# Optimization experiments

Measured on AMD Instinct MI355X. Metric: run time of the kernel, lower is better.

## Reference

```python
import jax, jax.numpy as jnp
import numpy as np

EPS = 1e-12


def setup_inputs() -> dict:
    key = jax.random.key(0)
    B, T, F = 16, 3000, 513
    hop, fs, t_psd = 256, 16000, 0.1
    alpha = jnp.array([1.0 - np.exp(-(hop / fs) / t_psd)], dtype=jnp.float32)
    x = jax.random.normal(key, (B, T, F), dtype=jnp.float32)
    running_mean = jnp.zeros((1, 1, F), dtype=jnp.float32)
    running_var = jnp.ones((1, 1, F), dtype=jnp.float32)
    return {"x": x, "running_mean": running_mean, "running_var": running_var, "alpha": alpha}


def reference(x, running_mean, running_var, alpha):
    # x: (B, T, F). EMA mean/var recurrence over T, then normalize.
    a = alpha.reshape(())
    B, T, F = x.shape
    m0 = jnp.broadcast_to(running_mean[:, 0, :], (B, F))
    v0 = jnp.broadcast_to(running_var[:, 0, :], (B, F))
    xt = jnp.swapaxes(x, 0, 1)  # (T, B, F)

    def step(carry, frame):
        m, v = carry
        m = (1.0 - a) * m + a * frame
        v = (1.0 - a) * v + a * (frame - m) ** 2
        return (m, v), (m, v)

    _, (means, vars_) = jax.lax.scan(step, (m0, v0), xt)
    means = jnp.swapaxes(means, 0, 1)  # (B, T, F)
    vars_ = jnp.swapaxes(vars_, 0, 1)
    return (x - means) / (vars_ * 4.0 + EPS)
```

## Files before the change

### kernel.cpp

```cpp
#include <hip/hip_runtime.h>


#define EPS 1e-12f

constexpr int B = 16;
constexpr int T = 3000;
constexpr int F = 513;
constexpr int CHUNK = 40;
constexpr int WARM = 64;
constexpr int NC = T / CHUNK;
constexpr int BT = 8;

__global__ __launch_bounds__(256, 8)
void OnlineNorm_11982958756550_kernel(
    const float* __restrict__ x,
    const float* __restrict__ rmean,
    const float* __restrict__ rvar,
    const float* __restrict__ alpha_p,
    float* __restrict__ out)
{
    const int idx = blockIdx.x * 256 + threadIdx.x;
    if (idx >= B * F) return;
    const int c = blockIdx.y;
    const int f = idx % F;
    const int b = idx / F;

    const float a = alpha_p[0];
    const float om_a = 1.0f - a;

    const int w_start = c * CHUNK;
    int t0 = w_start - WARM;
    float m, v;
    if (t0 <= 0) { t0 = 0; m = rmean[f]; v = rvar[f]; }
    else         { m = 0.0f; v = 0.0f; }

    const int nrows = w_start + CHUNK - t0;
    const int nb = nrows / BT;
    const int wb = (w_start - t0) / BT;

    const size_t cs = (size_t)BT * F;
    const float* lp = x   + (size_t)b * T * F + (size_t)t0 * F + f;
    const float* lend = lp + (size_t)nb * cs;
    float*       op = out + (size_t)b * T * F + (size_t)w_start * F + f;

    float bufA[BT], bufB[BT];

    #pragma unroll
    for (int i = 0; i < BT; ++i) bufA[i] = lp[(size_t)i * F];
    lp += cs;
    if (nb > 1) {
        #pragma unroll
        for (int i = 0; i < BT; ++i) bufB[i] = lp[(size_t)i * F];
        lp += cs;
    }

    auto process = [&](float (&buf)[BT], int k) {
        const bool is_out = (k >= wb);
        float r[BT];
        #pragma unroll
        for (int i = 0; i < BT; ++i) {
            const float e = buf[i] - m;
            m = fmaf(a, e, m);
            const float d = e * om_a;
            v = fmaf(a, fmaf(d, d, -v), v);
            if (is_out)
                r[i] = d * __builtin_amdgcn_rcpf(fmaf(v, 4.0f, EPS));
        }
        if (lp < lend) {
            #pragma unroll
            for (int i = 0; i < BT; ++i) buf[i] = lp[(size_t)i * F];
            lp += cs;
        }
        if (is_out) {
            #pragma unroll
            for (int i = 0; i < BT; ++i) op[(size_t)i * F] = r[i];
            op += cs;
        }
    };

    int k = 0;
    while (k < nb) {
        process(bufA, k); ++k;
        if (k >= nb) break;
        process(bufB, k); ++k;
    }
}

extern "C" void kernel_launch(void* const* d_in, const int* in_sizes, int n_in,
                              void* d_out, int out_size, void* d_ws, size_t ws_size,
                              hipStream_t stream) {
    const float* x      = (const float*)d_in[0];
    const float* rmean  = (const float*)d_in[1];
    const float* rvar   = (const float*)d_in[2];
    const float* alpha  = (const float*)d_in[3];
    float* out = (float*)d_out;

    const int bf = B * F;
    dim3 block(256);
    dim3 grid((bf + 255) / 256, NC);
    OnlineNorm_11982958756550_kernel<<<grid, block, 0, stream>>>(
        x, rmean, rvar, alpha, out);
}
```

Before: 208.3 us.

## Vectorize EMA normalization so each thread handles four features with 128-bit accesses

Remaps the kernel so each block covers one batch row and each of 128 threads processes four adjacent features through 16-byte loads and stores. The last thread also handles the leftover 513th feature as a scalar. Launch bounds and grid shape change to match. The aim is fewer memory instructions and more independent recurrences per thread, at the cost of far fewer resident threads for latency hiding, possibly unaligned vector accesses since F is odd, and extra serial work on the tail thread.

```diff
diff --git a/kernel.cpp b/kernel.cpp
--- a/kernel.cpp
+++ b/kernel.cpp
@@ -11,7 +11,16 @@
 constexpr int NC = T / CHUNK;
 constexpr int BT = 8;
 
-__global__ __launch_bounds__(256, 8)
+struct V4 { float v[4]; };
+
+__device__ __forceinline__ V4 ld4(const float* p) {
+    V4 r; __builtin_memcpy(&r, p, sizeof(V4)); return r;
+}
+__device__ __forceinline__ void st4(float* p, const V4& x) {
+    __builtin_memcpy(p, &x, sizeof(V4));
+}
+
+__global__ __launch_bounds__(128, 3)
 void OnlineNorm_11982958756550_kernel(
     const float* __restrict__ x,
     const float* __restrict__ rmean,
@@ -19,70 +28,113 @@
     const float* __restrict__ alpha_p,
     float* __restrict__ out)
 {
-    const int idx = blockIdx.x * 256 + threadIdx.x;
-    if (idx >= B * F) return;
+    const int b = blockIdx.x;
+    const int r = threadIdx.x;
+    const int f0 = r * 4;
+    const bool tail = (r == 127);
     const int c = blockIdx.y;
-    const int f = idx % F;
-    const int b = idx / F;
 
     const float a = alpha_p[0];
     const float om_a = 1.0f - a;
 
     const int w_start = c * CHUNK;
     int t0 = w_start - WARM;
-    float m, v;
-    if (t0 <= 0) { t0 = 0; m = rmean[f]; v = rvar[f]; }
-    else         { m = 0.0f; v = 0.0f; }
+    float m[4], v[4], ms, vs;
+    if (t0 <= 0) {
+        t0 = 0;
+        const V4 mm = ld4(rmean + f0);
+        const V4 vv = ld4(rvar + f0);
+        #pragma unroll
+        for (int j = 0; j < 4; ++j) { m[j] = mm.v[j]; v[j] = vv.v[j]; }
+        ms = rmean[F - 1]; vs = rvar[F - 1];
+    } else {
+        #pragma unroll
+        for (int j = 0; j < 4; ++j) { m[j] = 0.0f; v[j] = 0.0f; }
+        ms = 0.0f; vs = 0.0f;
+    }
 
     const int nrows = w_start + CHUNK - t0;
     const int nb = nrows / BT;
     const int wb = (w_start - t0) / BT;
 
     const size_t cs = (size_t)BT * F;
-    const float* lp = x   + (size_t)b * T * F + (size_t)t0 * F + f;
+    const size_t colbase = (size_t)b * T * F;
+    const float* lp   = x   + colbase + (size_t)t0 * F + f0;
+    const float* tlp  = x   + colbase + (size_t)t0 * F + (F - 1);
+    float*       op   = out + colbase + (size_t)w_start * F + f0;
+    float*       top  = out + colbase + (size_t)w_start * F + (F - 1);
     const float* lend = lp + (size_t)nb * cs;
-    float*       op = out + (size_t)b * T * F + (size_t)w_start * F + f;
 
-    float bufA[BT], bufB[BT];
+    V4 bufA[BT], bufB[BT];
+    float tbA[BT], tbB[BT];
 
     #pragma unroll
-    for (int i = 0; i < BT; ++i) bufA[i] = lp[(size_t)i * F];
-    lp += cs;
-    if (nb > 1) {
+    for (int i = 0; i < BT; ++i) bufA[i] = ld4(lp + (size_t)i * F);
+    if (tail) {
         #pragma unroll
-        for (int i = 0; i < BT; ++i) bufB[i] = lp[(size_t)i * F];
-        lp += cs;
+        for (int i = 0; i < BT; ++i) tbA[i] = tlp[(size_t)i * F];
     }
+    lp += cs; tlp += cs;
 
-    auto process = [&](float (&buf)[BT], int k) {
+    #pragma unroll
+    for (int i = 0; i < BT; ++i) bufB[i] = ld4(lp + (size_t)i * F);
+    if (tail) {
+        #pragma unroll
+        for (int i = 0; i < BT; ++i) tbB[i] = tlp[(size_t)i * F];
+    }
+    lp += cs; tlp += cs;
+
+    auto process = [&](V4 (&buf)[BT], float (&tb)[BT], int k) {
         const bool is_out = (k >= wb);
-        float r[BT];
+        V4 rr[BT]; float rt[BT];
         #pragma unroll
         for (int i = 0; i < BT; ++i) {
-            const float e = buf[i] - m;
-            m = fmaf(a, e, m);
-            const float d = e * om_a;
-            v = fmaf(a, fmaf(d, d, -v), v);
-            if (is_out)
-                r[i] = d * __builtin_amdgcn_rcpf(fmaf(v, 4.0f, EPS));
+            #pragma unroll
+            for (int j = 0; j < 4; ++j) {
+                const float e = buf[i].v[j] - m[j];
+                m[j] = fmaf(a, e, m[j]);
+                const float d = e * om_a;
+                v[j] = fmaf(a, fmaf(d, d, -v[j]), v[j]);
+                if (is_out)
+                    rr[i].v[j] = d * __builtin_amdgcn_rcpf(fmaf(v[j], 4.0f, EPS));
+            }
+        }
+        if (tail) {
+            #pragma unroll
+            for (int i = 0; i < BT; ++i) {
+                const float e = tb[i] - ms;
+                ms = fmaf(a, e, ms);
+                const float d = e * om_a;
+                vs = fmaf(a, fmaf(d, d, -vs), vs);
+                if (is_out)
+                    rt[i] = d * __builtin_amdgcn_rcpf(fmaf(vs, 4.0f, EPS));
+            }
         }
         if (lp < lend) {
             #pragma unroll
-            for (int i = 0; i < BT; ++i) buf[i] = lp[(size_t)i * F];
-            lp += cs;
+            for (int i = 0; i < BT; ++i) buf[i] = ld4(lp + (size_t)i * F);
+            if (tail) {
+                #pragma unroll
+                for (int i = 0; i < BT; ++i) tb[i] = tlp[(size_t)i * F];
+            }
+            lp += cs; tlp += cs;
         }
         if (is_out) {
             #pragma unroll
-            for (int i = 0; i < BT; ++i) op[(size_t)i * F] = r[i];
-            op += cs;
+            for (int i = 0; i < BT; ++i) st4(op + (size_t)i * F, rr[i]);
+            if (tail) {
+                #pragma unroll
+                for (int i = 0; i < BT; ++i) top[(size_t)i * F] = rt[i];
+            }
+            op += cs; top += cs;
         }
     };
 
     int k = 0;
     while (k < nb) {
-        process(bufA, k); ++k;
+        process(bufA, tbA, k); ++k;
         if (k >= nb) break;
-        process(bufB, k); ++k;
+        process(bufB, tbB, k); ++k;
     }
 }
 
@@ -95,9 +147,8 @@
     const float* alpha  = (const float*)d_in[3];
     float* out = (float*)d_out;
 
-    const int bf = B * F;
-    dim3 block(256);
-    dim3 grid((bf + 255) / 256, NC);
+    dim3 block(128);
+    dim3 grid(B, NC);
     OnlineNorm_11982958756550_kernel<<<grid, block, 0, stream>>>(
         x, rmean, rvar, alpha, out);
 }
```

New measurement: 223.2 us. 1.07x slower.

## Stage time-tiles through double-buffered LDS with one block per batch-chunk

Applied to the files above, without the earlier changes.

Each block now handles one (batch, chunk) pair. A tile of 8 frames x 513 features is staged into double-buffered shared memory using aligned float4 global loads, and each thread then runs the EMA recurrence for two features, plus the last feature on thread 255. This is meant to replace the unaligned strided per-thread loads with wide coalesced ones, and to overlap the next tile's fetch with compute. In exchange, the grid has about half as many blocks, each thread carries a longer serial chain, every step needs a block-wide barrier, and thread 255 does extra serial work. Launch bounds are relaxed to 4 blocks per SM.

```diff
diff --git a/kernel.cpp b/kernel.cpp
--- a/kernel.cpp
+++ b/kernel.cpp
@@ -10,8 +10,9 @@
 constexpr int WARM = 64;
 constexpr int NC = T / CHUNK;
 constexpr int BT = 8;
+constexpr int BWF = BT * F;
 
-__global__ __launch_bounds__(256, 8)
+__global__ __launch_bounds__(256, 4)
 void OnlineNorm_11982958756550_kernel(
     const float* __restrict__ x,
     const float* __restrict__ rmean,
@@ -19,70 +20,111 @@
     const float* __restrict__ alpha_p,
     float* __restrict__ out)
 {
-    const int idx = blockIdx.x * 256 + threadIdx.x;
-    if (idx >= B * F) return;
+    __shared__ float s[2][BWF];
+
+    const int b = blockIdx.x;
     const int c = blockIdx.y;
-    const int f = idx % F;
-    const int b = idx / F;
+    const int r = threadIdx.x;
 
     const float a = alpha_p[0];
     const float om_a = 1.0f - a;
 
     const int w_start = c * CHUNK;
     int t0 = w_start - WARM;
-    float m, v;
-    if (t0 <= 0) { t0 = 0; m = rmean[f]; v = rvar[f]; }
-    else         { m = 0.0f; v = 0.0f; }
-
+    const bool cold = (t0 <= 0);
+    if (cold) t0 = 0;
     const int nrows = w_start + CHUNK - t0;
     const int nb = nrows / BT;
     const int wb = (w_start - t0) / BT;
 
-    const size_t cs = (size_t)BT * F;
-    const float* lp = x   + (size_t)b * T * F + (size_t)t0 * F + f;
-    const float* lend = lp + (size_t)nb * cs;
-    float*       op = out + (size_t)b * T * F + (size_t)w_start * F + f;
-
-    float bufA[BT], bufB[BT];
-
-    #pragma unroll
-    for (int i = 0; i < BT; ++i) bufA[i] = lp[(size_t)i * F];
-    lp += cs;
-    if (nb > 1) {
-        #pragma unroll
-        for (int i = 0; i < BT; ++i) bufB[i] = lp[(size_t)i * F];
-        lp += cs;
+    float m0, v0, m1, v1, m2, v2;
+    if (cold) {
+        m0 = rmean[r];       v0 = rvar[r];
+        m1 = rmean[256 + r]; v1 = rvar[256 + r];
+        m2 = rmean[512];     v2 = rvar[512];
+    } else {
+        m0 = v0 = m1 = v1 = m2 = v2 = 0.0f;
     }
 
-    auto process = [&](float (&buf)[BT], int k) {
+    const size_t base = (size_t)b * T * F;
+    const float* gwin = x + base + (size_t)t0 * F;
+    float*       op   = out + base + (size_t)w_start * F;
+
+    float4 q0, q1, q2, q3;
+    float  tv;
+
+    auto stage_load = [&](int j) {
+        const float4* gp = (const float4*)(gwin + (size_t)j * BWF);
+        q0 = gp[r];
+        q1 = gp[r + 256];
+        q2 = gp[r + 512];
+        q3 = gp[r + 768];
+        tv = (r < 8) ? (gwin + (size_t)j * BWF)[4096 + r] : 0.0f;
+    };
+    auto stage_write = [&](int buf) {
+        float4* sp = (float4*)(s[buf]);
+        sp[r]       = q0;
+        sp[r + 256] = q1;
+        sp[r + 512] = q2;
+        sp[r + 768] = q3;
+        if (r < 8) s[buf][4096 + r] = tv;
+    };
+
+    stage_load(0);
+    stage_write(0);
+    __syncthreads();
+
+    int cur = 0;
+    for (int k = 0; k < nb; ++k) {
+        const bool more = (k + 1 < nb);
+        if (more) stage_load(k + 1);
         const bool is_out = (k >= wb);
-        float r[BT];
+        const float* sb = s[cur];
+        float r0[BT], r1[BT], r2[BT];
         #pragma unroll
         for (int i = 0; i < BT; ++i) {
-            const float e = buf[i] - m;
-            m = fmaf(a, e, m);
-            const float d = e * om_a;
-            v = fmaf(a, fmaf(d, d, -v), v);
-            if (is_out)
-                r[i] = d * __builtin_amdgcn_rcpf(fmaf(v, 4.0f, EPS));
+            const float x0 = sb[i * F + r];
+            const float x1 = sb[i * F + 256 + r];
+            const float e0 = x0 - m0;
+            m0 = fmaf(a, e0, m0);
+            const float d0 = e0 * om_a;
+            v0 = fmaf(a, fmaf(d0, d0, -v0), v0);
+            const float e1 = x1 - m1;
+            m1 = fmaf(a, e1, m1);
+            const float d1 = e1 * om_a;
+            v1 = fmaf(a, fmaf(d1, d1, -v1), v1);
+            if (is_out) {
+                r0[i] = d0 * __builtin_amdgcn_rcpf(fmaf(v0, 4.0f, EPS));
+                r1[i] = d1 * __builtin_amdgcn_rcpf(fmaf(v1, 4.0f, EPS));
+            }
         }
-        if (lp < lend) {
+        if (r == 255) {
             #pragma unroll
-            for (int i = 0; i < BT; ++i) buf[i] = lp[(size_t)i * F];
-            lp += cs;
+            for (int i = 0; i < BT; ++i) {
+                const float x2 = sb[i * F + 512];
+                const float e2 = x2 - m2;
+                m2 = fmaf(a, e2, m2);
+                const float d2 = e2 * om_a;
+                v2 = fmaf(a, fmaf(d2, d2, -v2), v2);
+                if (is_out)
+                    r2[i] = d2 * __builtin_amdgcn_rcpf(fmaf(v2, 4.0f, EPS));
+            }
         }
         if (is_out) {
             #pragma unroll
-            for (int i = 0; i < BT; ++i) op[(size_t)i * F] = r[i];
-            op += cs;
+            for (int i = 0; i < BT; ++i) {
+                op[(size_t)i * F + r]       = r0[i];
+                op[(size_t)i * F + 256 + r] = r1[i];
+            }
+            if (r == 255) {
+                #pragma unroll
+                for (int i = 0; i < BT; ++i) op[(size_t)i * F + 512] = r2[i];
+            }
+            op += (size_t)BT * F;
         }
-    };
-
-    int k = 0;
-    while (k < nb) {
-        process(bufA, k); ++k;
-        if (k >= nb) break;
-        process(bufB, k); ++k;
+        if (more) stage_write(cur ^ 1);
+        __syncthreads();
+        cur ^= 1;
     }
 }
 
@@ -95,9 +137,8 @@
     const float* alpha  = (const float*)d_in[3];
     float* out = (float*)d_out;
 
-    const int bf = B * F;
     dim3 block(256);
-    dim3 grid((bf + 255) / 256, NC);
+    dim3 grid(B, NC);
     OnlineNorm_11982958756550_kernel<<<grid, block, 0, stream>>>(
         x, rmean, rvar, alpha, out);
 }
```

After: 202.0 us. 3.0% less time.
